# Kernel tuning notes

Measured on AMD Instinct MI355X. Metric: run time of the kernel, lower is better.

The kernel has to match this reference:

```python
import jax, jax.numpy as jnp
import numpy as np

N_NODES = 256
BATCH = 262144
LIP_CONSTANT = 1.0
N_ITER = 20  # power-iteration steps for the Lipschitz (spectral) normalization


def _spectral_norm(W, n_iter=N_ITER):
    # Power iteration for the largest singular value of W.
    v = jnp.ones((W.shape[1],), W.dtype) / jnp.sqrt(jnp.asarray(W.shape[1], W.dtype))
    def body(v, _):
        u = W @ v
        u = u / (jnp.linalg.norm(u) + 1e-12)
        v = W.T @ u
        v = v / (jnp.linalg.norm(v) + 1e-12)
        return v, None
    v, _ = jax.lax.scan(body, v, None, length=n_iter)
    v = jax.lax.stop_gradient(v)
    return jnp.linalg.norm(W @ v) + 1e-12


def setup_inputs() -> dict:
    key = jax.random.key(0)
    kx, kw = jax.random.split(key)
    x = jax.random.normal(kx, (BATCH, N_NODES), dtype=jnp.float32)
    # learned weight of the square linearLipschitz layer (bias=False)
    W = jax.random.normal(kw, (N_NODES, N_NODES), dtype=jnp.float32) / jnp.sqrt(N_NODES)
    return {"x": x, "W": W}


def reference(x, W):
    # Lipschitz-constrained effective weight: W scaled so its spectral norm
    # equals lip_constant.
    W_eff = W * (LIP_CONSTANT / _spectral_norm(W))
    # Original loop: f_x[:, i] = layer(x @ U_i)[:, i] with U_i = I, U_i[i,i]=0.
    # => f_x[:, i] = sum_{j != i} x[:, j] * W_eff[i, j]
    # Collapsed: one GEMM minus the diagonal term.
    return x @ W_eff.T - x * jnp.diag(W_eff)[None, :]
```

## Files before the change

kernel.cpp:

```cpp
#include <hip/hip_runtime.h>
#include <stdint.h>

#define NN 256
#define BATCH 262144

typedef unsigned short ushort_t;
typedef __attribute__((ext_vector_type(8))) short short8_t;
typedef __attribute__((ext_vector_type(4))) float f32x4;

__device__ __forceinline__ ushort_t f2bf(float f) {
  uint32_t u = __float_as_uint(f);
  u += 0x7fffu + ((u >> 16) & 1u);
  return (ushort_t)(u >> 16);
}

__global__ __launch_bounds__(256) void gram_kernel(const float* __restrict__ W,
                                                   float* __restrict__ M) {
  int bi = blockIdx.x >> 4, bj = blockIdx.x & 15;
  int ti = threadIdx.x >> 4, tj = threadIdx.x & 15;
  int i = bi * 16 + ti, j = bj * 16 + tj;
  float acc = 0.f;
#pragma unroll 8
  for (int k = 0; k < NN; ++k) acc += W[k * NN + i] * W[k * NN + j];
  M[i * NN + j] = acc;
}

__global__ __launch_bounds__(256) void matsq_kernel(const float* __restrict__ A,
                                                    float* __restrict__ C) {
  int bi = blockIdx.x >> 4, bj = blockIdx.x & 15;
  int ti = threadIdx.x >> 4, tj = threadIdx.x & 15;
  int i = bi * 16 + ti, j = bj * 16 + tj;
  float acc = 0.f;
#pragma unroll 8
  for (int k = 0; k < NN; ++k) acc += A[i * NN + k] * A[k * NN + j];
  C[i * NN + j] = acc;
}

__global__ __launch_bounds__(1024) void power_kernel(const float* __restrict__ W,
                                                     const float* __restrict__ M,
                                                     const float* __restrict__ M4,
                                                     ushort_t* __restrict__ wz) {
  __shared__ float v_lds[NN];
  __shared__ float psum[4 * NN];
  __shared__ float red[16];
  __shared__ float scale_s;
  const int t = threadIdx.x;
  const int r = t >> 2, qc = t & 3;

  f32x4 Mreg[16];
#pragma unroll
  for (int j = 0; j < 16; ++j)
    Mreg[j] = *(const f32x4*)(M4 + r * NN + j * 16 + qc * 4);

  if (t < NN) v_lds[t] = 0.0625f;
  __syncthreads();

  for (int it = 0; it < 5; ++it) {
    float p = 0.f;
#pragma unroll
    for (int j = 0; j < 16; ++j) {
      f32x4 v4 = *(const f32x4*)(v_lds + j * 16 + qc * 4);
      p += Mreg[j].x * v4.x + Mreg[j].y * v4.y + Mreg[j].z * v4.z + Mreg[j].w * v4.w;
    }
    psum[qc * NN + r] = p;
    __syncthreads();
    if (t < NN)
      v_lds[t] = psum[t] + psum[NN + t] + psum[2 * NN + t] + psum[3 * NN + t];
    __syncthreads();
  }

  {
    float p = 0.f;
#pragma unroll
    for (int j = 0; j < 16; ++j) {
      f32x4 m4 = *(const f32x4*)(M + r * NN + j * 16 + qc * 4);
      f32x4 v4 = *(const f32x4*)(v_lds + j * 16 + qc * 4);
      p += m4.x * v4.x + m4.y * v4.y + m4.z * v4.z + m4.w * v4.w;
    }
    psum[qc * NN + r] = p;
    __syncthreads();
    float num = 0.f, den = 0.f;
    if (t < NN) {
      float y = psum[t] + psum[NN + t] + psum[2 * NN + t] + psum[3 * NN + t];
      float v = v_lds[t];
      num = v * y;
      den = v * v;
    }
#pragma unroll
    for (int off = 32; off > 0; off >>= 1) {
      num += __shfl_down(num, off);
      den += __shfl_down(den, off);
    }
    if (t < NN && (t & 63) == 0) {
      red[(t >> 6) * 2] = num;
      red[(t >> 6) * 2 + 1] = den;
    }
    __syncthreads();
    if (t == 0) {
      float n = red[0] + red[2] + red[4] + red[6];
      float d = red[1] + red[3] + red[5] + red[7];
      float sig = sqrtf(n / d) + 1e-12f;
      scale_s = 1.0f / sig;
    }
    __syncthreads();
  }
  const float scale = scale_s;

  for (int o = t; o < 8192; o += 1024) {
    int n = o >> 5;
    int koct = o & 31;
    int k0 = koct * 8;
    int kt = koct >> 2, kq = koct & 3;
    int kqs = kq ^ ((n >> 1) & 3);
    f32x4 a = *(const f32x4*)(W + n * NN + k0);
    f32x4 b = *(const f32x4*)(W + n * NN + k0 + 4);
    float f[8] = {a.x, a.y, a.z, a.w, b.x, b.y, b.z, b.w};
    short8_t pack;
#pragma unroll
    for (int e = 0; e < 8; ++e) {
      float val = (n == k0 + e) ? 0.f : f[e] * scale;
      pack[e] = (short)f2bf(val);
    }
    *(short8_t*)(wz + kt * 8192 + n * 32 + kqs * 8) = pack;
  }
}

__global__ __launch_bounds__(256, 3) void gemm_kernel(const float* __restrict__ x,
                                                      const ushort_t* __restrict__ wz,
                                                      float* __restrict__ out) {
  __shared__ __align__(16) ushort_t lsA[64 * 32];
  __shared__ __align__(16) ushort_t lsB[256 * 32];
  const int tid = threadIdx.x;
  const int wave = tid >> 6, lane = tid & 63;
  const int m0 = blockIdx.x * 64;
  const int m = lane & 15, q = lane >> 4;
  const int sw = (m >> 1) & 3;

  f32x4 acc[4][4];
  const f32x4 zero = {0.f, 0.f, 0.f, 0.f};
#pragma unroll
  for (int a = 0; a < 4; ++a)
#pragma unroll
    for (int b = 0; b < 4; ++b) acc[a][b] = zero;

  const int ar = tid >> 2;
  const int ak = tid & 3;
  const int achunk = ar * 4 + (ak ^ ((ar >> 1) & 3));
  const float* aptr = x + (m0 + ar) * NN + ak * 8;

  for (int kt = 0; kt < 8; ++kt) {
#pragma unroll
    for (int i = 0; i < 4; ++i) {
      const int cbase = i * 256 + wave * 64;
      __builtin_amdgcn_global_load_lds(
          (const __attribute__((address_space(1))) uint32_t*)(wz + kt * 8192 +
                                                              (cbase + lane) * 8),
          (__attribute__((address_space(3))) uint32_t*)(lsB + cbase * 8), 16, 0, 0);
    }
    f32x4 a0 = *(const f32x4*)(aptr + kt * 32);
    f32x4 a1 = *(const f32x4*)(aptr + kt * 32 + 4);
    short8_t av;
    av[0] = (short)f2bf(a0.x); av[1] = (short)f2bf(a0.y);
    av[2] = (short)f2bf(a0.z); av[3] = (short)f2bf(a0.w);
    av[4] = (short)f2bf(a1.x); av[5] = (short)f2bf(a1.y);
    av[6] = (short)f2bf(a1.z); av[7] = (short)f2bf(a1.w);
    *(short8_t*)(lsA + achunk * 8) = av;
    __syncthreads();

    short8_t af[4], bfrag[4];
#pragma unroll
    for (int mt = 0; mt < 4; ++mt) {
      int c = (mt * 16 + m) * 4 + (q ^ sw);
      af[mt] = *(const short8_t*)(lsA + c * 8);
    }
#pragma unroll
    for (int nt = 0; nt < 4; ++nt) {
      int c = (wave * 64 + nt * 16 + m) * 4 + (q ^ sw);
      bfrag[nt] = *(const short8_t*)(lsB + c * 8);
    }
#pragma unroll
    for (int mt = 0; mt < 4; ++mt)
#pragma unroll
      for (int nt = 0; nt < 4; ++nt)
        acc[mt][nt] = __builtin_amdgcn_mfma_f32_16x16x32_bf16(af[mt], bfrag[nt],
                                                              acc[mt][nt], 0, 0, 0);
    __syncthreads();
  }

#pragma unroll
  for (int mt = 0; mt < 4; ++mt) {
#pragma unroll
    for (int nt = 0; nt < 4; ++nt) {
      const int col = wave * 64 + nt * 16 + m;
      const int rowb = m0 + mt * 16 + q * 4;
#pragma unroll
      for (int e = 0; e < 4; ++e) out[(rowb + e) * NN + col] = acc[mt][nt][e];
    }
  }
}

extern "C" void kernel_launch(void* const* d_in, const int* in_sizes, int n_in,
                              void* d_out, int out_size, void* d_ws, size_t ws_size,
                              hipStream_t stream) {
  const float* x = (const float*)d_in[0];
  const float* W = (const float*)d_in[1];
  float* out = (float*)d_out;

  char* ws = (char*)d_ws;
  ushort_t* wz = (ushort_t*)ws;
  float* M = (float*)(ws + 131072);
  float* M2 = (float*)(ws + 131072 + 262144);
  float* M4 = (float*)(ws + 131072 + 2 * 262144);

  gram_kernel<<<256, 256, 0, stream>>>(W, M);
  matsq_kernel<<<256, 256, 0, stream>>>(M, M2);
  matsq_kernel<<<256, 256, 0, stream>>>(M2, M4);
  power_kernel<<<1, 1024, 0, stream>>>(W, M, M4, wz);
  gemm_kernel<<<BATCH / 64, 256, 0, stream>>>(x, wz, out);
}
```

Baseline: 494.7 us.

## Drop matrix-squaring kernels and LDS staging; load GEMM operands directly into registers

Removes the two matsq kernels and instead runs 20 plain power iterations on the Gram matrix inside the single-block power kernel, cutting two launches at the cost of a longer serial loop. The GEMM kernel no longer stages A and B through LDS with barriers. Each lane loads its x rows directly with nontemporal loads and converts them to bf16 in registers, and reads W fragments from a plain row-major layout. Output is written with nontemporal stores and occupancy is raised to 4 blocks per CU. The risk is redundant global loads of W and x across waves and uncoalesced per-lane access patterns in exchange for removing sync overhead.

```diff
diff --git a/kernel.cpp b/kernel.cpp
--- a/kernel.cpp
+++ b/kernel.cpp
@@ -25,20 +25,8 @@
   M[i * NN + j] = acc;
 }
 
-__global__ __launch_bounds__(256) void matsq_kernel(const float* __restrict__ A,
-                                                    float* __restrict__ C) {
-  int bi = blockIdx.x >> 4, bj = blockIdx.x & 15;
-  int ti = threadIdx.x >> 4, tj = threadIdx.x & 15;
-  int i = bi * 16 + ti, j = bj * 16 + tj;
-  float acc = 0.f;
-#pragma unroll 8
-  for (int k = 0; k < NN; ++k) acc += A[i * NN + k] * A[k * NN + j];
-  C[i * NN + j] = acc;
-}
-
 __global__ __launch_bounds__(1024) void power_kernel(const float* __restrict__ W,
                                                      const float* __restrict__ M,
-                                                     const float* __restrict__ M4,
                                                      ushort_t* __restrict__ wz) {
   __shared__ float v_lds[NN];
   __shared__ float psum[4 * NN];
@@ -50,12 +38,12 @@
   f32x4 Mreg[16];
 #pragma unroll
   for (int j = 0; j < 16; ++j)
-    Mreg[j] = *(const f32x4*)(M4 + r * NN + j * 16 + qc * 4);
+    Mreg[j] = *(const f32x4*)(M + r * NN + j * 16 + qc * 4);
 
   if (t < NN) v_lds[t] = 0.0625f;
   __syncthreads();
 
-  for (int it = 0; it < 5; ++it) {
+  for (int it = 0; it < 21; ++it) {
     float p = 0.f;
 #pragma unroll
     for (int j = 0; j < 16; ++j) {
@@ -64,54 +52,42 @@
     }
     psum[qc * NN + r] = p;
     __syncthreads();
-    if (t < NN)
-      v_lds[t] = psum[t] + psum[NN + t] + psum[2 * NN + t] + psum[3 * NN + t];
-    __syncthreads();
+    if (it < 20) {
+      if (t < NN)
+        v_lds[t] = psum[t] + psum[NN + t] + psum[2 * NN + t] + psum[3 * NN + t];
+      __syncthreads();
+    }
   }
 
-  {
-    float p = 0.f;
+  float num = 0.f, den = 0.f;
+  if (t < NN) {
+    float y = psum[t] + psum[NN + t] + psum[2 * NN + t] + psum[3 * NN + t];
+    float v = v_lds[t];
+    num = v * y;
+    den = v * v;
+  }
 #pragma unroll
-    for (int j = 0; j < 16; ++j) {
-      f32x4 m4 = *(const f32x4*)(M + r * NN + j * 16 + qc * 4);
-      f32x4 v4 = *(const f32x4*)(v_lds + j * 16 + qc * 4);
-      p += m4.x * v4.x + m4.y * v4.y + m4.z * v4.z + m4.w * v4.w;
-    }
-    psum[qc * NN + r] = p;
-    __syncthreads();
-    float num = 0.f, den = 0.f;
-    if (t < NN) {
-      float y = psum[t] + psum[NN + t] + psum[2 * NN + t] + psum[3 * NN + t];
-      float v = v_lds[t];
-      num = v * y;
-      den = v * v;
-    }
-#pragma unroll
-    for (int off = 32; off > 0; off >>= 1) {
-      num += __shfl_down(num, off);
-      den += __shfl_down(den, off);
-    }
-    if (t < NN && (t & 63) == 0) {
-      red[(t >> 6) * 2] = num;
-      red[(t >> 6) * 2 + 1] = den;
-    }
-    __syncthreads();
-    if (t == 0) {
-      float n = red[0] + red[2] + red[4] + red[6];
-      float d = red[1] + red[3] + red[5] + red[7];
-      float sig = sqrtf(n / d) + 1e-12f;
-      scale_s = 1.0f / sig;
-    }
-    __syncthreads();
+  for (int off = 32; off > 0; off >>= 1) {
+    num += __shfl_down(num, off);
+    den += __shfl_down(den, off);
   }
+  if (t < NN && (t & 63) == 0) {
+    red[(t >> 6) * 2] = num;
+    red[(t >> 6) * 2 + 1] = den;
+  }
+  __syncthreads();
+  if (t == 0) {
+    float n = red[0] + red[2] + red[4] + red[6];
+    float d = red[1] + red[3] + red[5] + red[7];
+    float sig = sqrtf(n / d) + 1e-12f;
+    scale_s = 1.0f / sig;
+  }
+  __syncthreads();
   const float scale = scale_s;
 
   for (int o = t; o < 8192; o += 1024) {
     int n = o >> 5;
-    int koct = o & 31;
-    int k0 = koct * 8;
-    int kt = koct >> 2, kq = koct & 3;
-    int kqs = kq ^ ((n >> 1) & 3);
+    int k0 = (o & 31) * 8;
     f32x4 a = *(const f32x4*)(W + n * NN + k0);
     f32x4 b = *(const f32x4*)(W + n * NN + k0 + 4);
     float f[8] = {a.x, a.y, a.z, a.w, b.x, b.y, b.z, b.w};
@@ -121,20 +97,17 @@
       float val = (n == k0 + e) ? 0.f : f[e] * scale;
       pack[e] = (short)f2bf(val);
     }
-    *(short8_t*)(wz + kt * 8192 + n * 32 + kqs * 8) = pack;
+    *(short8_t*)(wz + n * NN + k0) = pack;
   }
 }
 
-__global__ __launch_bounds__(256, 3) void gemm_kernel(const float* __restrict__ x,
+__global__ __launch_bounds__(256, 4) void gemm_kernel(const float* __restrict__ x,
                                                       const ushort_t* __restrict__ wz,
                                                       float* __restrict__ out) {
-  __shared__ __align__(16) ushort_t lsA[64 * 32];
-  __shared__ __align__(16) ushort_t lsB[256 * 32];
   const int tid = threadIdx.x;
   const int wave = tid >> 6, lane = tid & 63;
+  const int m = lane & 15, q = lane >> 4;
   const int m0 = blockIdx.x * 64;
-  const int m = lane & 15, q = lane >> 4;
-  const int sw = (m >> 1) & 3;
 
   f32x4 acc[4][4];
   const f32x4 zero = {0.f, 0.f, 0.f, 0.f};
@@ -143,48 +116,35 @@
 #pragma unroll
     for (int b = 0; b < 4; ++b) acc[a][b] = zero;
 
-  const int ar = tid >> 2;
-  const int ak = tid & 3;
-  const int achunk = ar * 4 + (ak ^ ((ar >> 1) & 3));
-  const float* aptr = x + (m0 + ar) * NN + ak * 8;
+  const float* xbase = x + (m0 + m) * NN + q * 8;
+  const ushort_t* wbase = wz + (wave * 64 + m) * NN + q * 8;
 
   for (int kt = 0; kt < 8; ++kt) {
+    short8_t bfrag[4];
 #pragma unroll
-    for (int i = 0; i < 4; ++i) {
-      const int cbase = i * 256 + wave * 64;
-      __builtin_amdgcn_global_load_lds(
-          (const __attribute__((address_space(1))) uint32_t*)(wz + kt * 8192 +
-                                                              (cbase + lane) * 8),
-          (__attribute__((address_space(3))) uint32_t*)(lsB + cbase * 8), 16, 0, 0);
-    }
-    f32x4 a0 = *(const f32x4*)(aptr + kt * 32);
-    f32x4 a1 = *(const f32x4*)(aptr + kt * 32 + 4);
-    short8_t av;
-    av[0] = (short)f2bf(a0.x); av[1] = (short)f2bf(a0.y);
-    av[2] = (short)f2bf(a0.z); av[3] = (short)f2bf(a0.w);
-    av[4] = (short)f2bf(a1.x); av[5] = (short)f2bf(a1.y);
-    av[6] = (short)f2bf(a1.z); av[7] = (short)f2bf(a1.w);
-    *(short8_t*)(lsA + achunk * 8) = av;
-    __syncthreads();
+    for (int nt = 0; nt < 4; ++nt)
+      bfrag[nt] = *(const short8_t*)(wbase + nt * 16 * NN + kt * 32);
 
-    short8_t af[4], bfrag[4];
+    short8_t af[4];
 #pragma unroll
     for (int mt = 0; mt < 4; ++mt) {
-      int c = (mt * 16 + m) * 4 + (q ^ sw);
-      af[mt] = *(const short8_t*)(lsA + c * 8);
+      const float* p = xbase + (mt * 16) * NN + kt * 32;
+      f32x4 a0 = __builtin_nontemporal_load((const f32x4*)p);
+      f32x4 a1 = __builtin_nontemporal_load((const f32x4*)(p + 4));
+      short8_t av;
+      av[0] = (short)f2bf(a0.x); av[1] = (short)f2bf(a0.y);
+      av[2] = (short)f2bf(a0.z); av[3] = (short)f2bf(a0.w);
+      av[4] = (short)f2bf(a1.x); av[5] = (short)f2bf(a1.y);
+      av[6] = (short)f2bf(a1.z); av[7] = (short)f2bf(a1.w);
+      af[mt] = av;
     }
-#pragma unroll
-    for (int nt = 0; nt < 4; ++nt) {
-      int c = (wave * 64 + nt * 16 + m) * 4 + (q ^ sw);
-      bfrag[nt] = *(const short8_t*)(lsB + c * 8);
-    }
+
 #pragma unroll
     for (int mt = 0; mt < 4; ++mt)
 #pragma unroll
       for (int nt = 0; nt < 4; ++nt)
         acc[mt][nt] = __builtin_amdgcn_mfma_f32_16x16x32_bf16(af[mt], bfrag[nt],
                                                               acc[mt][nt], 0, 0, 0);
-    __syncthreads();
   }
 
 #pragma unroll
@@ -194,7 +154,8 @@
       const int col = wave * 64 + nt * 16 + m;
       const int rowb = m0 + mt * 16 + q * 4;
 #pragma unroll
-      for (int e = 0; e < 4; ++e) out[(rowb + e) * NN + col] = acc[mt][nt][e];
+      for (int e = 0; e < 4; ++e)
+        __builtin_nontemporal_store(acc[mt][nt][e], out + (rowb + e) * NN + col);
     }
   }
 }
@@ -209,12 +170,8 @@
   char* ws = (char*)d_ws;
   ushort_t* wz = (ushort_t*)ws;
   float* M = (float*)(ws + 131072);
-  float* M2 = (float*)(ws + 131072 + 262144);
-  float* M4 = (float*)(ws + 131072 + 2 * 262144);
 
   gram_kernel<<<256, 256, 0, stream>>>(W, M);
-  matsq_kernel<<<256, 256, 0, stream>>>(M, M2);
-  matsq_kernel<<<256, 256, 0, stream>>>(M2, M4);
-  power_kernel<<<1, 1024, 0, stream>>>(W, M, M4, wz);
+  power_kernel<<<1, 1024, 0, stream>>>(W, M, wz);
   gemm_kernel<<<BATCH / 64, 256, 0, stream>>>(x, wz, out);
 }
```

Result: slower. 658.6 us (+33.1%).
